# Kernel tuning notes

Measured on AMD Instinct MI355X. Metric: run time of the kernel, lower is better.

The kernel has to match this reference:

```python
import jax, jax.numpy as jnp
import numpy as np

B, S, D, K = 16384, 50, 512, 5  # batch, pred_horizon(=steps), dec_units, components_n
H = S  # time_stamp width equals pred_horizon


def setup_inputs() -> dict:
    key = jax.random.key(0)
    ks = jax.random.split(key, 13)
    sc = 0.05
    f32 = jnp.float32
    return {
        "conditions": jax.random.normal(ks[0], (B, S, 3), f32),
        "state_h": jax.random.normal(ks[1], (B, D), f32),
        "state_c": jax.random.normal(ks[2], (B, D), f32),
        # merger LSTM (input = enc_h[D] ++ cond[3])
        "W_m": jax.random.normal(ks[3], (D + 3, 4 * D), f32) * sc,
        "U_m": jax.random.normal(ks[4], (D, 4 * D), f32) * sc,
        "b_m": jnp.zeros((4 * D,), f32),
        # merger MDN heads packed: [alphas|mus_long|sigmas_long|mus_lat|sigmas_lat|rhos]
        "Wh_m": jax.random.normal(ks[5], (D + H, 6 * K), f32) * sc,
        "bh_m": jnp.zeros((6 * K,), f32),
        # yielder LSTM
        "W_y": jax.random.normal(ks[6], (D + 3, 4 * D), f32) * sc,
        "U_y": jax.random.normal(ks[7], (D, 4 * D), f32) * sc,
        "b_y": jnp.zeros((4 * D,), f32),
        # yielder MDN heads packed: [alphas|mus_long|sigmas_long]
        "Wh_y": jax.random.normal(ks[8], (D + H, 3 * K), f32) * sc,
        "bh_y": jnp.zeros((3 * K,), f32),
    }


def _lstm_step(x, h, c, W, U, b):
    # Keras LSTM gate order: i, f, g(cell), o
    z = x @ W + h @ U + b
    i, f, g, o = jnp.split(z, 4, axis=-1)
    c2 = jax.nn.sigmoid(f) * c + jax.nn.sigmoid(i) * jnp.tanh(g)
    h2 = jax.nn.sigmoid(o) * jnp.tanh(c2)
    return h2, c2


def reference(conditions, state_h, state_c, W_m, U_m, b_m, Wh_m, bh_m,
              W_y, U_y, b_y, Wh_y, bh_y):
    # time_stamp[s] = ones in [:s+1] (lower-triangular)
    time_stamp = jnp.tril(jnp.ones((S, H), conditions.dtype))
    enc_h = state_h  # re-fed every step, [B, D]
    # With teacher_percent=1.0 both merger and yielder step conditions are
    # conditions[:, t, :3] at step t (step 0 also uses t=0).
    conds_t = jnp.transpose(conditions, (1, 0, 2))  # [S, B, 3]

    def step(carry, xs):
        h_m, c_m, h_y, c_y = carry
        cond_t, ts = xs  # [B,3], [H]
        x_in = jnp.concatenate([enc_h, cond_t], axis=-1)  # [B, D+3]
        ts_b = jnp.broadcast_to(ts, (h_m.shape[0], H))
        # merger vehicle
        h_m, c_m = _lstm_step(x_in, h_m, c_m, W_m, U_m, b_m)
        feat_m = jnp.concatenate([h_m, ts_b], axis=-1)  # [B, D+H]
        zm = feat_m @ Wh_m + bh_m
        a, ml, sl, mlt, slt, r = jnp.split(zm, 6, axis=-1)
        pm = jnp.concatenate([jax.nn.softmax(a, axis=-1), ml, jnp.exp(sl),
                              mlt, jnp.exp(slt), jnp.tanh(r)], axis=-1)  # [B,30]
        # yielder vehicle
        h_y, c_y = _lstm_step(x_in, h_y, c_y, W_y, U_y, b_y)
        feat_y = jnp.concatenate([h_y, ts_b], axis=-1)
        zy = feat_y @ Wh_y + bh_y
        ay, mly, sly = jnp.split(zy, 3, axis=-1)
        py = jnp.concatenate([jax.nn.softmax(ay, axis=-1), mly, jnp.exp(sly)], axis=-1)  # [B,15]
        return (h_m, c_m, h_y, c_y), (pm, py)

    carry0 = (state_h, state_c, state_h, state_c)
    _, (param_m, param_y) = jax.lax.scan(step, carry0, (conds_t, time_stamp))
    param_m = jnp.transpose(param_m, (1, 0, 2))  # [B, S, 30]
    param_y = jnp.transpose(param_y, (1, 0, 2))  # [B, S, 15]
    return param_m, param_y
```

## Files before the change

### kernel.cpp

```cpp
#include <hip/hip_runtime.h>

typedef __bf16 bf16;
typedef __attribute__((ext_vector_type(8))) __bf16 bf16x8;
typedef __attribute__((ext_vector_type(4))) __bf16 bf16x4;
typedef __attribute__((ext_vector_type(4))) float f32x4;
typedef __attribute__((ext_vector_type(4))) int i32x4;

#define B_TOT 16384
#define SEQ 50
#define DH 512
#define ZW 2048
#define NT 16

#define MFMA16(a, b, c) __builtin_amdgcn_mfma_f32_16x16x32_bf16(a, b, c, 0, 0, 0)

__device__ __forceinline__ float fsigm(float x) {
    return __fdividef(1.0f, 1.0f + __expf(-x));
}
__device__ __forceinline__ float ftanh(float x) {
    float e = __expf(2.0f * x);
    return 1.0f - __fdividef(2.0f, e + 1.0f);
}


__global__ void init_state(const float* __restrict__ sh,
                           bf16* __restrict__ h0m, bf16* __restrict__ h0y) {
    size_t i = (size_t)blockIdx.x * 256 + threadIdx.x;
    int row = i >> 9, k = i & 511;
    size_t off = (((size_t)(row >> 4) * 16 + (k >> 5)) * 64 + ((k >> 3) & 3) * 16 +
                  (row & 15)) * 8 + (k & 7);
    bf16 hb = (bf16)sh[i];
    h0m[off] = hb;
    h0y[off] = hb;
}

__global__ void build_c3(const float* __restrict__ src,
                         float* __restrict__ dM, float* __restrict__ dY) {
    size_t i = (size_t)blockIdx.x * 256 + threadIdx.x;
    int row = i >> 9, hcol = i & 511;
    float v = src[i];
    size_t o = ((size_t)(row >> 2) * 512 + hcol) * 4 + (row & 3);
    dM[o] = v;
    dY[o] = v;
}

__device__ __forceinline__ int orig_col(int colp) {
    return ((colp >> 4) & 3) * 512 + ((colp >> 6) << 4) + (colp & 15);
}

__global__ void reorder_weights(const float* __restrict__ Um, const float* __restrict__ Uy,
                                const float* __restrict__ Wm, const float* __restrict__ Wy,
                                bf16* __restrict__ UtM, bf16* __restrict__ UtY,
                                bf16* __restrict__ WtM, bf16* __restrict__ WtY) {
    int idx = blockIdx.x * 256 + threadIdx.x;
    int which = idx >> 20;
    int r = idx & ((1 << 20) - 1);
    int colp = r >> 9, k = r & 511;
    int orig = orig_col(colp);
    const float* src = which == 0 ? Um : which == 1 ? Uy : which == 2 ? Wm : Wy;
    bf16* dst = which == 0 ? UtM : which == 1 ? UtY : which == 2 ? WtM : WtY;
    int cb = colp >> 4, fr = colp & 15;
    int kt = k >> 5, fq = (k >> 3) & 3, e = k & 7;
    int lane = fq * 16 + fr;
    dst[(((size_t)(cb * 16 + kt) * 64 + lane) << 3) + e] = (bf16)src[(size_t)k * ZW + orig];
}

__global__ void build_wc2(const float* __restrict__ Wm, const float* __restrict__ Wy,
                          float* __restrict__ Wc2M, float* __restrict__ Wc2Y) {
    int idx = blockIdx.x * 256 + threadIdx.x;
    if (idx >= 2 * 512 * 12) return;
    int which = idx / 6144;
    int r2 = idx % 6144;
    int hcol = r2 / 12, rg = r2 % 12;
    int r = rg >> 2, g = rg & 3;
    const float* src = which ? Wy : Wm;
    float* dst = which ? Wc2Y : Wc2M;
    dst[hcol * 12 + rg] = src[(size_t)(512 + r) * ZW + g * 512 + hcol];
}

__global__ void cond_transpose(const float* __restrict__ cond, float* __restrict__ condT4) {
    int idx = blockIdx.x * 256 + threadIdx.x;
    if (idx >= SEQ * B_TOT) return;
    int t = idx / B_TOT, row = idx % B_TOT;
    const float* s = cond + ((size_t)row * SEQ + t) * 3;
    f32x4 v = {s[0], s[1], s[2], 0.f};
    *(f32x4*)(condT4 + (size_t)idx * 4) = v;
}

__global__ void build_heads(const float* __restrict__ Whm, const float* __restrict__ bhm,
                            const float* __restrict__ Why, const float* __restrict__ bhy,
                            bf16* __restrict__ WhmT, bf16* __restrict__ WhyT,
                            float* __restrict__ tscm, float* __restrict__ tscy) {
    int i = blockIdx.x * 256 + threadIdx.x;
    const int N1 = 32 * 512, N2 = 16 * 512, N3 = SEQ * 32, N4 = SEQ * 16;
    if (i < N1) {
        int n = i >> 9, k = i & 511;
        WhmT[i] = (bf16)(n < 30 ? Whm[k * 30 + n] : 0.f);
    } else if (i < N1 + N2) {
        int j = i - N1;
        int n = j >> 9, k = j & 511;
        WhyT[j] = (bf16)(n < 15 ? Why[k * 15 + n] : 0.f);
    } else if (i < N1 + N2 + N3) {
        int j = i - (N1 + N2);
        int tt = j >> 5, col = j & 31;
        float v = 0.f;
        if (col < 30) {
            v = bhm[col];
            for (int s = 0; s <= tt; ++s) v += Whm[(512 + s) * 30 + col];
        }
        tscm[j] = v;
    } else if (i < N1 + N2 + N3 + N4) {
        int j = i - (N1 + N2 + N3);
        int tt = j >> 4, col = j & 15;
        float v = 0.f;
        if (col < 15) {
            v = bhy[col];
            for (int s = 0; s <= tt; ++s) v += Why[(512 + s) * 15 + col];
        }
        tscy[j] = v;
    }
}


#define WAIT_VM(n)                                                  \
    do {                                                            \
        asm volatile("s_waitcnt vmcnt(" #n ")" ::: "memory");       \
        __builtin_amdgcn_sched_barrier(0);                          \
    } while (0)

template <int MODE>
__global__ __launch_bounds__(256, 3) void gemm_step(
    const bf16* __restrict__ Am, const bf16* __restrict__ Ay,
    const bf16* __restrict__ BtM, const bf16* __restrict__ BtY,
    const bf16* __restrict__ xwM, const bf16* __restrict__ xwY,
    const float* __restrict__ Wc2M, const float* __restrict__ Wc2Y,
    const float* __restrict__ biasM, const float* __restrict__ biasY,
    float* __restrict__ cM, float* __restrict__ cY,
    bf16* __restrict__ hoM, bf16* __restrict__ hoY,
    bf16* __restrict__ xoM, bf16* __restrict__ xoY,
    const float* __restrict__ condT4, int t) {
    const int tid = threadIdx.x;
    const int wave = tid >> 6, lane = tid & 63;
    const int lin = blockIdx.y * 128 + blockIdx.x;
    const int xcd = lin & 7, jj2 = lin >> 3;
    const int bx = xcd * 16 + (jj2 >> 4);
    const int by = jj2 & 15;
    const int brow = bx * 128;
    const int bz = blockIdx.z;
    const bf16* A = bz ? Ay : Am;
    const bf16* Bt = bz ? BtY : BtM;

    const int fr = lane & 15, fq = lane >> 4;
    const int wr = wave >> 1, wc = wave & 1;

    const uint64_t abase =
        (uint64_t)(const char*)A + (uint64_t)(bx * 8 + wr * 4) * 16384 + lane * 16;
    const uint64_t bbase =
        (uint64_t)(const char*)Bt + (uint64_t)(by * 8 + wc * 4) * 16384 + lane * 16;

    f32x4 acc[4][4];
#pragma unroll
    for (int m = 0; m < 4; ++m)
#pragma unroll
        for (int n = 0; n < 4; ++n) acc[m][n] = (f32x4){0.f, 0.f, 0.f, 0.f};

    i32x4 afr[2][4], bfr[2][4];

#define AGLOAD(bank, kts)                                                         \
    do {                                                                          \
        uint64_t _a = abase + (uint64_t)(kts) * 1024;                             \
        asm volatile("global_load_dwordx4 %0, %1, off"                            \
                     : "=&v"(afr[bank][0]) : "v"(_a) : "memory");                 \
        asm volatile("global_load_dwordx4 %0, %1, off"                            \
                     : "=&v"(afr[bank][1]) : "v"(_a + 16384) : "memory");         \
        asm volatile("global_load_dwordx4 %0, %1, off"                            \
                     : "=&v"(afr[bank][2]) : "v"(_a + 32768) : "memory");         \
        asm volatile("global_load_dwordx4 %0, %1, off"                            \
                     : "=&v"(afr[bank][3]) : "v"(_a + 49152) : "memory");         \
    } while (0)
#define BGLOAD(bank, kts)                                                         \
    do {                                                                          \
        uint64_t _b = bbase + (uint64_t)(kts) * 1024;                             \
        asm volatile("global_load_dwordx4 %0, %1, off"                            \
                     : "=&v"(bfr[bank][0]) : "v"(_b) : "memory");                 \
        asm volatile("global_load_dwordx4 %0, %1, off"                            \
                     : "=&v"(bfr[bank][1]) : "v"(_b + 16384) : "memory");         \
        asm volatile("global_load_dwordx4 %0, %1, off"                            \
                     : "=&v"(bfr[bank][2]) : "v"(_b + 32768) : "memory");         \
        asm volatile("global_load_dwordx4 %0, %1, off"                            \
                     : "=&v"(bfr[bank][3]) : "v"(_b + 49152) : "memory");         \
    } while (0)

    AGLOAD(0, 0);
    BGLOAD(0, 0);
    AGLOAD(1, 1);
    BGLOAD(1, 1);

#pragma unroll
    for (int kt = 0; kt < NT; ++kt) {
        if (kt < NT - 1) {
            WAIT_VM(8);
        } else {
            WAIT_VM(0);
        }
        __builtin_amdgcn_s_setprio(1);
#pragma unroll
        for (int m = 0; m < 4; ++m)
#pragma unroll
            for (int n = 0; n < 4; ++n)
                acc[m][n] = MFMA16(__builtin_bit_cast(bf16x8, afr[kt & 1][m]),
                                   __builtin_bit_cast(bf16x8, bfr[kt & 1][n]), acc[m][n]);
        __builtin_amdgcn_s_setprio(0);
        __builtin_amdgcn_sched_barrier(0);
        if (kt + 2 < NT) {
            AGLOAD(kt & 1, kt + 2);
            BGLOAD(kt & 1, kt + 2);
        }
    }
#undef AGLOAD
#undef BGLOAD

    const int jb = by * 2 + wc;
    const int hcol = jb * 16 + fr;
    const int rowbase = brow + wr * 64 + fq * 4;
    const int rb0 = (rowbase >> 2);

    if (MODE == 0) {
        const float* bias = bz ? biasY : biasM;
        bf16* XO = bz ? xoY : xoM;
        float b0 = bias[hcol], b1 = bias[512 + hcol], b2 = bias[1024 + hcol],
              b3 = bias[1536 + hcol];
#pragma unroll
        for (int m = 0; m < 4; ++m) {
            bf16x8 v0, v1;
#pragma unroll
            for (int j = 0; j < 2; ++j) {
                v0[j * 4 + 0] = (bf16)(acc[m][0][j] + b0);
                v0[j * 4 + 1] = (bf16)(acc[m][1][j] + b1);
                v0[j * 4 + 2] = (bf16)(acc[m][2][j] + b2);
                v0[j * 4 + 3] = (bf16)(acc[m][3][j] + b3);
            }
#pragma unroll
            for (int j = 2; j < 4; ++j) {
                v1[(j - 2) * 4 + 0] = (bf16)(acc[m][0][j] + b0);
                v1[(j - 2) * 4 + 1] = (bf16)(acc[m][1][j] + b1);
                v1[(j - 2) * 4 + 2] = (bf16)(acc[m][2][j] + b2);
                v1[(j - 2) * 4 + 3] = (bf16)(acc[m][3][j] + b3);
            }
            bf16* o = XO + ((size_t)(rb0 + m * 4) * 512 + hcol) * 16;
            *(bf16x8*)(o) = v0;
            *(bf16x8*)(o + 8) = v1;
        }
    } else {
        float* Cb = bz ? cY : cM;
        bf16* Ho = bz ? hoY : hoM;
        const bf16* xw = bz ? xwY : xwM;
        const float* Wc2 = bz ? Wc2Y : Wc2M;
        f32x4 wcv0 = *(const f32x4*)(Wc2 + hcol * 12);
        f32x4 wcv1 = *(const f32x4*)(Wc2 + hcol * 12 + 4);
        f32x4 wcv2 = *(const f32x4*)(Wc2 + hcol * 12 + 8);
        const int ktc = jb >> 1;
        const int fqp = (jb & 1) * 2 + (fr >> 3);
        bf16* hob = Ho + (((size_t)((brow >> 4) + wr * 4) * 16 + ktc) * 64 + fqp * 16 +
                          fq * 4) * 8 + (fr & 7);
#pragma unroll
        for (int m = 0; m < 4; ++m) {
            const size_t co = ((size_t)(rb0 + m * 4) * 512 + hcol);
            const bf16* xp = xw + co * 16;
            bf16x8 xv0 = *(const bf16x8*)(xp);
            bf16x8 xv1 = *(const bf16x8*)(xp + 8);
            f32x4 cvm = *(const f32x4*)(Cb + co * 4);
            const int row0 = rowbase + m * 16;
            f32x4 cd[4];
#pragma unroll
            for (int j = 0; j < 4; ++j)
                cd[j] = *(const f32x4*)(condT4 + ((size_t)t * B_TOT + row0 + j) * 4);
            f32x4 cnew;
            bf16* hom = hob + (size_t)m * 16 * 64 * 8;
#pragma unroll
            for (int j = 0; j < 4; ++j) {
                float z[4];
#pragma unroll
                for (int g = 0; g < 4; ++g) {
                    float xwv = (j < 2) ? (float)xv0[j * 4 + g] : (float)xv1[(j - 2) * 4 + g];
                    z[g] = acc[m][g][j] + xwv + cd[j][0] * wcv0[g] + cd[j][1] * wcv1[g] +
                           cd[j][2] * wcv2[g];
                }
                float ii = fsigm(z[0]);
                float ff = fsigm(z[1]);
                float gg = ftanh(z[2]);
                float oo = fsigm(z[3]);
                float cn = ff * cvm[j] + ii * gg;
                cnew[j] = cn;
                hom[j * 8] = (bf16)(oo * ftanh(cn));
            }
            *(f32x4*)(Cb + co * 4) = cnew;
        }
    }
}

__global__ __launch_bounds__(128) void heads_step(
    const bf16* __restrict__ hm, const bf16* __restrict__ hy,
    const bf16* __restrict__ WhmT, const bf16* __restrict__ WhyT,
    const float* __restrict__ tscm, const float* __restrict__ tscy,
    float* __restrict__ out, int t) {
    __shared__ float zbuf[2 * 768];
    const int tid = threadIdx.x, wave = tid >> 6, lane = tid & 63;
    const int fr = lane & 15, fq = lane >> 4;
    const int rbase = blockIdx.x * 32 + wave * 16;
    const int rg = rbase >> 4;

    f32x4 am0 = {0.f, 0.f, 0.f, 0.f}, am1 = {0.f, 0.f, 0.f, 0.f}, ay0 = {0.f, 0.f, 0.f, 0.f};

    for (int kt = 0; kt < 16; ++kt) {
        const size_t ao = ((size_t)(rg * 16 + kt) * 64 + lane) * 8;
        bf16x8 a0 = *(const bf16x8*)(hm + ao);
        bf16x8 y0 = *(const bf16x8*)(hy + ao);
        const int k0 = kt * 32;
        const size_t bo = (size_t)fr * DH + k0 + fq * 8;
        bf16x8 b0 = *(const bf16x8*)(WhmT + bo);
        bf16x8 b1 = *(const bf16x8*)(WhmT + bo + 16 * DH);
        bf16x8 yb = *(const bf16x8*)(WhyT + bo);
        am0 = MFMA16(a0, b0, am0);
        am1 = MFMA16(a0, b1, am1);
        ay0 = MFMA16(y0, yb, ay0);
    }

    float* zm = zbuf + wave * 768;
    float* zy = zm + 512;
#pragma unroll
    for (int j = 0; j < 4; ++j) {
        int rl = fq * 4 + j;
        zm[rl * 32 + fr] = am0[j] + tscm[t * 32 + fr];
        zm[rl * 32 + 16 + fr] = am1[j] + tscm[t * 32 + 16 + fr];
        zy[rl * 16 + fr] = ay0[j] + tscy[t * 16 + fr];
    }
    __syncthreads();

    const int r = lane & 15;
    const size_t grow = (size_t)rbase + r;
    if (lane < 16) {
        float z[30];
#pragma unroll
        for (int i = 0; i < 30; ++i) z[i] = zm[r * 32 + i];
        float* o = out + (grow * SEQ + t) * 30;
        float mx = z[0];
#pragma unroll
        for (int i = 1; i < 5; ++i) mx = fmaxf(mx, z[i]);
        float e[5], s = 0.f;
#pragma unroll
        for (int i = 0; i < 5; ++i) {
            e[i] = __expf(z[i] - mx);
            s += e[i];
        }
        float inv = __fdividef(1.f, s);
#pragma unroll
        for (int i = 0; i < 5; ++i) o[i] = e[i] * inv;
#pragma unroll
        for (int i = 5; i < 10; ++i) o[i] = z[i];
#pragma unroll
        for (int i = 10; i < 15; ++i) o[i] = __expf(z[i]);
#pragma unroll
        for (int i = 15; i < 20; ++i) o[i] = z[i];
#pragma unroll
        for (int i = 20; i < 25; ++i) o[i] = __expf(z[i]);
#pragma unroll
        for (int i = 25; i < 30; ++i) o[i] = ftanh(z[i]);
    } else if (lane < 32) {
        float z[15];
#pragma unroll
        for (int i = 0; i < 15; ++i) z[i] = zy[r * 16 + i];
        float* o = out + (size_t)B_TOT * SEQ * 30 + (grow * SEQ + t) * 15;
        float mx = z[0];
#pragma unroll
        for (int i = 1; i < 5; ++i) mx = fmaxf(mx, z[i]);
        float e[5], s = 0.f;
#pragma unroll
        for (int i = 0; i < 5; ++i) {
            e[i] = __expf(z[i] - mx);
            s += e[i];
        }
        float inv = __fdividef(1.f, s);
#pragma unroll
        for (int i = 0; i < 5; ++i) o[i] = e[i] * inv;
#pragma unroll
        for (int i = 5; i < 10; ++i) o[i] = z[i];
#pragma unroll
        for (int i = 10; i < 15; ++i) o[i] = __expf(z[i]);
    }
}

extern "C" void kernel_launch(void* const* d_in, const int* in_sizes, int n_in,
                              void* d_out, int out_size, void* d_ws, size_t ws_size,
                              hipStream_t stream) {
    const float* cond = (const float*)d_in[0];
    const float* sh = (const float*)d_in[1];
    const float* sc = (const float*)d_in[2];
    const float* Wm = (const float*)d_in[3];
    const float* Um = (const float*)d_in[4];
    const float* bm = (const float*)d_in[5];
    const float* Whm = (const float*)d_in[6];
    const float* bhm = (const float*)d_in[7];
    const float* Wy = (const float*)d_in[8];
    const float* Uy = (const float*)d_in[9];
    const float* by_ = (const float*)d_in[10];
    const float* Why = (const float*)d_in[11];
    const float* bhy = (const float*)d_in[12];
    float* out = (float*)d_out;

    char* p = (char*)d_ws;
    auto take = [&](size_t bytes) {
        char* r = p;
        p += (bytes + 255) & ~(size_t)255;
        return r;
    };
    bf16* UtM = (bf16*)take((size_t)ZW * DH * 2);
    bf16* UtY = (bf16*)take((size_t)ZW * DH * 2);
    bf16* WtM = (bf16*)take((size_t)ZW * DH * 2);
    bf16* WtY = (bf16*)take((size_t)ZW * DH * 2);
    float* Wc2M = (float*)take(512 * 12 * 4);
    float* Wc2Y = (float*)take(512 * 12 * 4);
    bf16* WhmT = (bf16*)take(32 * DH * 2);
    bf16* WhyT = (bf16*)take(16 * DH * 2);
    float* tscm = (float*)take(SEQ * 32 * 4);
    float* tscy = (float*)take(SEQ * 16 * 4);
    float* condT4 = (float*)take((size_t)SEQ * B_TOT * 4 * 4);
    bf16* xwM = (bf16*)take((size_t)B_TOT * ZW * 2);
    bf16* xwY = (bf16*)take((size_t)B_TOT * ZW * 2);
    bf16* hM0 = (bf16*)take((size_t)B_TOT * DH * 2);
    bf16* hM1 = (bf16*)take((size_t)B_TOT * DH * 2);
    bf16* hY0 = (bf16*)take((size_t)B_TOT * DH * 2);
    bf16* hY1 = (bf16*)take((size_t)B_TOT * DH * 2);
    float* cMb = (float*)take((size_t)B_TOT * DH * 4);
    float* cYb = (float*)take((size_t)B_TOT * DH * 4);
    bf16* hM[2] = {hM0, hM1};
    bf16* hY[2] = {hY0, hY1};

    init_state<<<(B_TOT * DH) / 256, 256, 0, stream>>>(sh, hM0, hY0);
    build_c3<<<(B_TOT * DH) / 256, 256, 0, stream>>>(sc, cMb, cYb);
    reorder_weights<<<(4 * ZW * DH) / 256, 256, 0, stream>>>(Um, Uy, Wm, Wy, UtM, UtY, WtM, WtY);
    build_wc2<<<(2 * 512 * 12 + 255) / 256, 256, 0, stream>>>(Wm, Wy, Wc2M, Wc2Y);
    cond_transpose<<<(SEQ * B_TOT + 255) / 256, 256, 0, stream>>>(cond, condT4);
    build_heads<<<(32 * 512 + 16 * 512 + SEQ * 32 + SEQ * 16 + 255) / 256, 256, 0, stream>>>(
        Whm, bhm, Why, bhy, WhmT, WhyT, tscm, tscy);

    dim3 ggrid(B_TOT / 128, ZW / 128, 2);
    gemm_step<0><<<ggrid, 256, 0, stream>>>(hM0, hM0, WtM, WtY, nullptr, nullptr,
                                            nullptr, nullptr, bm, by_, nullptr, nullptr,
                                            nullptr, nullptr, xwM, xwY, condT4, 0);

    for (int t = 0; t < SEQ; ++t) {
        const int a = t & 1, b = (t + 1) & 1;
        gemm_step<1><<<ggrid, 256, 0, stream>>>(hM[a], hY[a], UtM, UtY, xwM, xwY,
                                                Wc2M, Wc2Y, nullptr, nullptr, cMb, cYb,
                                                hM[b], hY[b], nullptr, nullptr, condT4, t);
        heads_step<<<B_TOT / 32, 128, 0, stream>>>(hM[b], hY[b], WhmT, WhyT, tscm, tscy, out, t);
    }
}
```

Measured before the change: 7.164 ms.

## Fuse decoder timesteps into a persistent cooperative kernel with grid sync

Replaces the per-timestep launches of the gate GEMM and heads kernels with one cooperative persistent kernel of 768 blocks. Each block loops over work items per step and the steps are separated by grid.sync, removing about 100 kernel launches. The heads for step t-1 now run in the same phase as the GEMM for step t, so the two overlap. In exchange the tile-to-XCD swizzle is dropped, heads tiles grow to 256 threads, and the grid barriers plus the fixed block count could lower GEMM efficiency. A fallback to non-persistent launches is kept in case the cooperative launch fails.

Result: slower. 20.01 ms (+179.4%).

```diff
diff --git a/kernel.cpp b/kernel.cpp
--- a/kernel.cpp
+++ b/kernel.cpp
@@ -1,4 +1,7 @@
 #include <hip/hip_runtime.h>
+#include <hip/hip_cooperative_groups.h>
+
+namespace cg = cooperative_groups;
 
 typedef __bf16 bf16;
 typedef __attribute__((ext_vector_type(8))) __bf16 bf16x8;
@@ -11,6 +14,9 @@
 #define DH 512
 #define ZW 2048
 #define NT 16
+#define NBLK 768
+#define NGEMM 4096
+#define NITEM 4352
 
 #define MFMA16(a, b, c) __builtin_amdgcn_mfma_f32_16x16x32_bf16(a, b, c, 0, 0, 0)
 
@@ -122,6 +128,18 @@
 }
 
 
+struct DecP {
+    bf16 *hM0, *hM1, *hY0, *hY1;
+    const bf16 *UtM, *UtY, *WtM, *WtY;
+    bf16 *xwM, *xwY;
+    const float *Wc2M, *Wc2Y, *bm, *by_;
+    float *cM, *cY;
+    const float* condT4;
+    const bf16 *WhmT, *WhyT;
+    const float *tscm, *tscy;
+    float* out;
+};
+
 #define WAIT_VM(n)                                                  \
     do {                                                            \
         asm volatile("s_waitcnt vmcnt(" #n ")" ::: "memory");       \
@@ -129,26 +147,23 @@
     } while (0)
 
 template <int MODE>
-__global__ __launch_bounds__(256, 3) void gemm_step(
-    const bf16* __restrict__ Am, const bf16* __restrict__ Ay,
-    const bf16* __restrict__ BtM, const bf16* __restrict__ BtY,
-    const bf16* __restrict__ xwM, const bf16* __restrict__ xwY,
-    const float* __restrict__ Wc2M, const float* __restrict__ Wc2Y,
-    const float* __restrict__ biasM, const float* __restrict__ biasY,
-    float* __restrict__ cM, float* __restrict__ cY,
-    bf16* __restrict__ hoM, bf16* __restrict__ hoY,
-    bf16* __restrict__ xoM, bf16* __restrict__ xoY,
-    const float* __restrict__ condT4, int t) {
+__device__ __forceinline__ void gemm_item(const DecP& P, int item, int t) {
     const int tid = threadIdx.x;
     const int wave = tid >> 6, lane = tid & 63;
-    const int lin = blockIdx.y * 128 + blockIdx.x;
-    const int xcd = lin & 7, jj2 = lin >> 3;
-    const int bx = xcd * 16 + (jj2 >> 4);
-    const int by = jj2 & 15;
+    const int bz = item >> 11;
+    const int lin = item & 2047;
+    const int bx = lin & 127, by = lin >> 7;
     const int brow = bx * 128;
-    const int bz = blockIdx.z;
-    const bf16* A = bz ? Ay : Am;
-    const bf16* Bt = bz ? BtY : BtM;
+
+    const bf16* A;
+    const bf16* Bt;
+    if (MODE == 0) {
+        A = P.hM0;
+        Bt = bz ? P.WtY : P.WtM;
+    } else {
+        A = bz ? ((t & 1) ? P.hY1 : P.hY0) : ((t & 1) ? P.hM1 : P.hM0);
+        Bt = bz ? P.UtY : P.UtM;
+    }
 
     const int fr = lane & 15, fq = lane >> 4;
     const int wr = wave >> 1, wc = wave & 1;
@@ -226,8 +241,8 @@
     const int rb0 = (rowbase >> 2);
 
     if (MODE == 0) {
-        const float* bias = bz ? biasY : biasM;
-        bf16* XO = bz ? xoY : xoM;
+        const float* bias = bz ? P.by_ : P.bm;
+        bf16* XO = bz ? P.xwY : P.xwM;
         float b0 = bias[hcol], b1 = bias[512 + hcol], b2 = bias[1024 + hcol],
               b3 = bias[1536 + hcol];
 #pragma unroll
@@ -252,10 +267,11 @@
             *(bf16x8*)(o + 8) = v1;
         }
     } else {
-        float* Cb = bz ? cY : cM;
-        bf16* Ho = bz ? hoY : hoM;
-        const bf16* xw = bz ? xwY : xwM;
-        const float* Wc2 = bz ? Wc2Y : Wc2M;
+        float* Cb = bz ? P.cY : P.cM;
+        bf16* Ho = bz ? (((t + 1) & 1) ? P.hY1 : P.hY0)
+                      : (((t + 1) & 1) ? P.hM1 : P.hM0);
+        const bf16* xw = bz ? P.xwY : P.xwM;
+        const float* Wc2 = bz ? P.Wc2Y : P.Wc2M;
         f32x4 wcv0 = *(const f32x4*)(Wc2 + hcol * 12);
         f32x4 wcv1 = *(const f32x4*)(Wc2 + hcol * 12 + 4);
         f32x4 wcv2 = *(const f32x4*)(Wc2 + hcol * 12 + 8);
@@ -274,7 +290,7 @@
             f32x4 cd[4];
 #pragma unroll
             for (int j = 0; j < 4; ++j)
-                cd[j] = *(const f32x4*)(condT4 + ((size_t)t * B_TOT + row0 + j) * 4);
+                cd[j] = *(const f32x4*)(P.condT4 + ((size_t)t * B_TOT + row0 + j) * 4);
             f32x4 cnew;
             bf16* hom = hob + (size_t)m * 16 * 64 * 8;
 #pragma unroll
@@ -299,16 +315,14 @@
     }
 }
 
-__global__ __launch_bounds__(128) void heads_step(
-    const bf16* __restrict__ hm, const bf16* __restrict__ hy,
-    const bf16* __restrict__ WhmT, const bf16* __restrict__ WhyT,
-    const float* __restrict__ tscm, const float* __restrict__ tscy,
-    float* __restrict__ out, int t) {
-    __shared__ float zbuf[2 * 768];
+__device__ __forceinline__ void heads_item(const DecP& P, float* zbuf, int hb, int th) {
     const int tid = threadIdx.x, wave = tid >> 6, lane = tid & 63;
     const int fr = lane & 15, fq = lane >> 4;
-    const int rbase = blockIdx.x * 32 + wave * 16;
+    const int rbase = hb * 64 + wave * 16;
     const int rg = rbase >> 4;
+    const int a = (th + 1) & 1;
+    const bf16* hm = a ? P.hM1 : P.hM0;
+    const bf16* hy = a ? P.hY1 : P.hY0;
 
     f32x4 am0 = {0.f, 0.f, 0.f, 0.f}, am1 = {0.f, 0.f, 0.f, 0.f}, ay0 = {0.f, 0.f, 0.f, 0.f};
 
@@ -318,9 +332,9 @@
         bf16x8 y0 = *(const bf16x8*)(hy + ao);
         const int k0 = kt * 32;
         const size_t bo = (size_t)fr * DH + k0 + fq * 8;
-        bf16x8 b0 = *(const bf16x8*)(WhmT + bo);
-        bf16x8 b1 = *(const bf16x8*)(WhmT + bo + 16 * DH);
-        bf16x8 yb = *(const bf16x8*)(WhyT + bo);
+        bf16x8 b0 = *(const bf16x8*)(P.WhmT + bo);
+        bf16x8 b1 = *(const bf16x8*)(P.WhmT + bo + 16 * DH);
+        bf16x8 yb = *(const bf16x8*)(P.WhyT + bo);
         am0 = MFMA16(a0, b0, am0);
         am1 = MFMA16(a0, b1, am1);
         ay0 = MFMA16(y0, yb, ay0);
@@ -331,9 +345,9 @@
 #pragma unroll
     for (int j = 0; j < 4; ++j) {
         int rl = fq * 4 + j;
-        zm[rl * 32 + fr] = am0[j] + tscm[t * 32 + fr];
-        zm[rl * 32 + 16 + fr] = am1[j] + tscm[t * 32 + 16 + fr];
-        zy[rl * 16 + fr] = ay0[j] + tscy[t * 16 + fr];
+        zm[rl * 32 + fr] = am0[j] + P.tscm[th * 32 + fr];
+        zm[rl * 32 + 16 + fr] = am1[j] + P.tscm[th * 32 + 16 + fr];
+        zy[rl * 16 + fr] = ay0[j] + P.tscy[th * 16 + fr];
     }
     __syncthreads();
 
@@ -343,7 +357,7 @@
         float z[30];
 #pragma unroll
         for (int i = 0; i < 30; ++i) z[i] = zm[r * 32 + i];
-        float* o = out + (grow * SEQ + t) * 30;
+        float* o = P.out + (grow * SEQ + th) * 30;
         float mx = z[0];
 #pragma unroll
         for (int i = 1; i < 5; ++i) mx = fmaxf(mx, z[i]);
@@ -370,7 +384,7 @@
         float z[15];
 #pragma unroll
         for (int i = 0; i < 15; ++i) z[i] = zy[r * 16 + i];
-        float* o = out + (size_t)B_TOT * SEQ * 30 + (grow * SEQ + t) * 15;
+        float* o = P.out + (size_t)B_TOT * SEQ * 30 + (grow * SEQ + th) * 15;
         float mx = z[0];
 #pragma unroll
         for (int i = 1; i < 5; ++i) mx = fmaxf(mx, z[i]);
@@ -387,6 +401,37 @@
         for (int i = 5; i < 10; ++i) o[i] = z[i];
 #pragma unroll
         for (int i = 10; i < 15; ++i) o[i] = __expf(z[i]);
+    }
+    __syncthreads();
+}
+
+__device__ __forceinline__ void run_item(const DecP& P, float* zbuf, int item, int t) {
+    if (item < NGEMM) {
+        if (t < 0)
+            gemm_item<0>(P, item, 0);
+        else if (t < SEQ)
+            gemm_item<1>(P, item, t);
+    } else if (item < NITEM) {
+        if (t >= 1) heads_item(P, zbuf, item - NGEMM, t - 1);
+    }
+}
+
+template <bool PERSIST>
+__global__ __launch_bounds__(256, 3) void decoder_step(DecP P, int t0, int itemOff) {
+    __shared__ float zbuf[4 * 768];
+    if constexpr (PERSIST) {
+        cg::grid_group grid = cg::this_grid();
+        const int blk = blockIdx.x;
+        for (int t = -1; t <= SEQ; ++t) {
+            for (int r = 0; r < 6; ++r) {
+                const int it = r * NBLK + blk;
+                if (it < NITEM) run_item(P, zbuf, it, t);
+            }
+            __threadfence();
+            grid.sync();
+        }
+    } else {
+        run_item(P, zbuf, blockIdx.x + itemOff, t0);
     }
 }
 
@@ -433,8 +478,6 @@
     bf16* hY1 = (bf16*)take((size_t)B_TOT * DH * 2);
     float* cMb = (float*)take((size_t)B_TOT * DH * 4);
     float* cYb = (float*)take((size_t)B_TOT * DH * 4);
-    bf16* hM[2] = {hM0, hM1};
-    bf16* hY[2] = {hY0, hY1};
 
     init_state<<<(B_TOT * DH) / 256, 256, 0, stream>>>(sh, hM0, hY0);
     build_c3<<<(B_TOT * DH) / 256, 256, 0, stream>>>(sc, cMb, cYb);
@@ -444,16 +487,39 @@
     build_heads<<<(32 * 512 + 16 * 512 + SEQ * 32 + SEQ * 16 + 255) / 256, 256, 0, stream>>>(
         Whm, bhm, Why, bhy, WhmT, WhyT, tscm, tscy);
 
-    dim3 ggrid(B_TOT / 128, ZW / 128, 2);
-    gemm_step<0><<<ggrid, 256, 0, stream>>>(hM0, hM0, WtM, WtY, nullptr, nullptr,
-                                            nullptr, nullptr, bm, by_, nullptr, nullptr,
-                                            nullptr, nullptr, xwM, xwY, condT4, 0);
-
-    for (int t = 0; t < SEQ; ++t) {
-        const int a = t & 1, b = (t + 1) & 1;
-        gemm_step<1><<<ggrid, 256, 0, stream>>>(hM[a], hY[a], UtM, UtY, xwM, xwY,
-                                                Wc2M, Wc2Y, nullptr, nullptr, cMb, cYb,
-                                                hM[b], hY[b], nullptr, nullptr, condT4, t);
-        heads_step<<<B_TOT / 32, 128, 0, stream>>>(hM[b], hY[b], WhmT, WhyT, tscm, tscy, out, t);
-    }
-}
+    DecP P;
+    P.hM0 = hM0;
+    P.hM1 = hM1;
+    P.hY0 = hY0;
+    P.hY1 = hY1;
+    P.UtM = UtM;
+    P.UtY = UtY;
+    P.WtM = WtM;
+    P.WtY = WtY;
+    P.xwM = xwM;
+    P.xwY = xwY;
+    P.Wc2M = Wc2M;
+    P.Wc2Y = Wc2Y;
+    P.bm = bm;
+    P.by_ = by_;
+    P.cM = cMb;
+    P.cY = cYb;
+    P.condT4 = condT4;
+    P.WhmT = WhmT;
+    P.WhyT = WhyT;
+    P.tscm = tscm;
+    P.tscy = tscy;
+    P.out = out;
+
+    int zero = 0;
+    void* kargs[] = {(void*)&P, (void*)&zero, (void*)&zero};
+    hipError_t err = hipLaunchCooperativeKernel(
+        reinterpret_cast<void*>(&decoder_step<true>), dim3(NBLK), dim3(256), kargs, 0, stream);
+    if (err != hipSuccess) {
+        (void)hipGetLastError();
+        decoder_step<false><<<NGEMM, 256, 0, stream>>>(P, -1, 0);
+        for (int t = 0; t < SEQ; ++t)
+            decoder_step<false><<<NITEM, 256, 0, stream>>>(P, t, 0);
+        decoder_step<false><<<NITEM - NGEMM, 256, 0, stream>>>(P, SEQ, NGEMM);
+    }
+}
```
